# Optimization experiments

Hardware: AMD Instinct MI355X
Metric: run time of the kernel (lower is better)

The kernel has to match this reference:

```python
import jax, jax.numpy as jnp
import numpy as np

B, T, C, NH = 8, 1024, 768, 12
HD = C // NH


def setup_inputs() -> dict:
    key = jax.random.key(0)
    k1, k2, k3, k4, k5 = jax.random.split(key, 5)
    s = 0.02
    return {
        "x": jax.random.normal(k1, (B, T, C), dtype=jnp.float32),
        "w_attn": jax.random.normal(k2, (C, 3 * C), dtype=jnp.float32) * s,
        "b_attn": jax.random.normal(k3, (3 * C,), dtype=jnp.float32) * s,
        "w_proj": jax.random.normal(k4, (C, C), dtype=jnp.float32) * s,
        "b_proj": jax.random.normal(k5, (C,), dtype=jnp.float32) * s,
    }


def reference(x, w_attn, b_attn, w_proj, b_proj):
    Bv, Tv, Cv = x.shape
    # fused QKV projection
    qkv = jnp.einsum('btc,cd->btd', x, w_attn) + b_attn  # [B,T,3C]
    q, k, v = jnp.split(qkv, 3, axis=-1)
    # [B, NH, T, HD]
    q = q.reshape(Bv, Tv, NH, HD).transpose(0, 2, 1, 3)
    k = k.reshape(Bv, Tv, NH, HD).transpose(0, 2, 1, 3)
    v = v.reshape(Bv, Tv, NH, HD).transpose(0, 2, 1, 3)
    scale = 1.0 / np.sqrt(HD).astype(np.float32)
    att = jnp.einsum('bhqd,bhkd->bhqk', q, k) * scale  # [B,NH,T,T]
    causal = jnp.tril(jnp.ones((Tv, Tv), dtype=bool))
    att = jnp.where(causal, att, -jnp.inf)
    att = jax.nn.softmax(att, axis=-1)
    y = jnp.einsum('bhqk,bhkd->bhqd', att, v)  # [B,NH,T,HD]
    y = y.transpose(0, 2, 1, 3).reshape(Bv, Tv, Cv)
    return jnp.einsum('btc,cd->btd', y, w_proj) + b_proj
```

## Files before the change

kernel.cpp:

```cpp
#include <hip/hip_runtime.h>

constexpr int kB  = 8;
constexpr int kT  = 1024;
constexpr int kC  = 768;
constexpr int kNH = 12;
constexpr int kHD = 64;
constexpr int kM  = kB * kT;
constexpr int k3C = 3 * kC;

using bf16x8 = __attribute__((ext_vector_type(8))) __bf16;
using f32x4  = __attribute__((ext_vector_type(4))) float;

__device__ __forceinline__ float bf2f(unsigned short u) {
    union { unsigned int i; float f; } v;
    v.i = ((unsigned int)u) << 16;
    return v.f;
}

__device__ __forceinline__ unsigned short f2bf(float f) {
    union { float f; unsigned int u; } v; v.f = f;
    unsigned int r = v.u + 0x7fffu + ((v.u >> 16) & 1u);
    return (unsigned short)(r >> 16);
}

__device__ __forceinline__ void async16(const void* g, void* l) {
    __builtin_amdgcn_global_load_lds(
        (__attribute__((address_space(1))) void*)g,
        (__attribute__((address_space(3))) void*)l, 16, 0, 0);
}

__device__ __forceinline__ void wait_vm0() {
    __builtin_amdgcn_s_waitcnt(0x0F70);
}


__global__ __launch_bounds__(256) void cvt_bf16_kernel(
    const float* __restrict__ in, unsigned short* __restrict__ out)
{
    const int i = blockIdx.x * 256 + threadIdx.x;
    const float4 v = ((const float4*)in)[i];
    ushort4 o;
    o.x = f2bf(v.x); o.y = f2bf(v.y); o.z = f2bf(v.z); o.w = f2bf(v.w);
    ((ushort4*)out)[i] = o;
}

__global__ __launch_bounds__(256) void transpose_cvt_kernel(
    const float* __restrict__ W, unsigned short* __restrict__ Wt, int K, int N)
{
    __shared__ float tile[32][33];
    const int tx = threadIdx.x & 31, ty = threadIdx.x >> 5;
    const int n0 = blockIdx.x * 32, k0 = blockIdx.y * 32;
    #pragma unroll
    for (int i = 0; i < 4; ++i)
        tile[ty + i * 8][tx] = W[(size_t)(k0 + ty + i * 8) * N + n0 + tx];
    __syncthreads();
    #pragma unroll
    for (int i = 0; i < 4; ++i)
        Wt[(size_t)(n0 + ty + i * 8) * K + k0 + tx] = f2bf(tile[tx][ty + i * 8]);
}

__global__ __launch_bounds__(256) void vtrans_kernel(
    const unsigned short* __restrict__ qkv, unsigned short* __restrict__ VT)
{
    __shared__ unsigned short tile[64][72];
    const int tid = threadIdx.x;
    const int bh = blockIdx.x >> 4;
    const int b = bh / kNH, h = bh % kNH;
    const int tt = (blockIdx.x & 15) * 64;
    const int row = tid >> 2;
    const int c0  = (tid & 3) * 16;
    const unsigned short* src =
        qkv + (size_t)(b * kT + tt + row) * k3C + 2 * kC + h * kHD + c0;
    *(uint4*)&tile[row][c0]     = *(const uint4*)src;
    *(uint4*)&tile[row][c0 + 8] = *(const uint4*)(src + 8);
    __syncthreads();
    const int d  = tid >> 2;
    const int t8 = (tid & 3) * 16;
    unsigned short tmp[16];
    #pragma unroll
    for (int i = 0; i < 16; ++i) tmp[i] = tile[t8 + i][d];
    unsigned short* dst = VT + ((size_t)bh * kHD + d) * kT + tt + t8;
    *(uint4*)dst       = *(uint4*)&tmp[0];
    *(uint4*)(dst + 8) = *(uint4*)&tmp[8];
}

template<bool OUT_BF16>
__global__ __launch_bounds__(256) void gemm_mfma_kernel(
    const unsigned short* __restrict__ A, int lda,
    const unsigned short* __restrict__ Bt,
    const float* __restrict__ bias,
    void* __restrict__ outv, int N, int K)
{
    alignas(16) __shared__ unsigned short As[16 * 512];
    alignas(16) __shared__ unsigned short Bs[16 * 512];

    const int tid  = threadIdx.x;
    const int w    = tid >> 6;
    const int lane = tid & 63;
    const int wr = w >> 1, wc = w & 1;
    const int m0 = blockIdx.y * 128, n0 = blockIdx.x * 128;

    const int fr = lane & 15;
    const int fk = (lane >> 4) * 8;

    f32x4 acc[4][4];
    #pragma unroll
    for (int i = 0; i < 4; ++i)
        #pragma unroll
        for (int j = 0; j < 4; ++j) {
            f32x4 z = {0.f, 0.f, 0.f, 0.f};
            acc[i][j] = z;
        }

    for (int kt = 0; kt < K; kt += 64) {
        #pragma unroll
        for (int t = 0; t < 4; ++t) {
            const int fa = w * 4 + t;
            const int ki = fa >> 3, si = fa & 7;
            const unsigned short* ga =
                A + (size_t)(m0 + si * 16 + fr) * lda + kt + ki * 32 + fk;
            async16(ga, &As[fa * 512]);
            const unsigned short* gb =
                Bt + (size_t)(n0 + si * 16 + fr) * K + kt + ki * 32 + fk;
            async16(gb, &Bs[fa * 512]);
        }
        wait_vm0();
        __syncthreads();

        #pragma unroll
        for (int ki = 0; ki < 2; ++ki) {
            bf16x8 a[4], b[4];
            #pragma unroll
            for (int i = 0; i < 4; ++i)
                a[i] = *(const bf16x8*)&As[(ki * 8 + wr * 4 + i) * 512 + lane * 8];
            #pragma unroll
            for (int j = 0; j < 4; ++j)
                b[j] = *(const bf16x8*)&Bs[(ki * 8 + wc * 4 + j) * 512 + lane * 8];
            #pragma unroll
            for (int i = 0; i < 4; ++i)
                #pragma unroll
                for (int j = 0; j < 4; ++j)
                    acc[i][j] = __builtin_amdgcn_mfma_f32_16x16x32_bf16(
                        a[i], b[j], acc[i][j], 0, 0, 0);
        }
        __syncthreads();
    }

    const int quad  = lane >> 4;
    const int col16 = lane & 15;
    float biasv[4];
    #pragma unroll
    for (int j = 0; j < 4; ++j)
        biasv[j] = bias[n0 + wc * 64 + j * 16 + col16];

    #pragma unroll
    for (int i = 0; i < 4; ++i) {
        #pragma unroll
        for (int r = 0; r < 4; ++r) {
            const int row = m0 + wr * 64 + i * 16 + quad * 4 + r;
            #pragma unroll
            for (int j = 0; j < 4; ++j) {
                const int col = n0 + wc * 64 + j * 16 + col16;
                const float v = acc[i][j][r] + biasv[j];
                if (OUT_BF16)
                    ((unsigned short*)outv)[(size_t)row * N + col] = f2bf(v);
                else
                    ((float*)outv)[(size_t)row * N + col] = v;
            }
        }
    }
}

__global__ __launch_bounds__(256) void attn_mfma_kernel(
    const unsigned short* __restrict__ qkv,
    const unsigned short* __restrict__ VT,
    unsigned short* __restrict__ y)
{
    alignas(16) __shared__ unsigned short Qf[8 * 512];
    alignas(16) __shared__ unsigned short Kf[8 * 512];
    alignas(16) __shared__ unsigned short Vf[8 * 512];
    alignas(16) __shared__ unsigned short Pf[8 * 512];

    const int tid  = threadIdx.x;
    const int w    = tid >> 6;
    const int lane = tid & 63;
    const int quad = lane >> 4, l15 = lane & 15;
    const int bh = blockIdx.x >> 4;
    const int b  = bh / kNH, h = bh % kNH;
    const int t0 = (15 - (blockIdx.x & 15)) * 64;

    {
        const unsigned short* g0 =
            qkv + (size_t)(b * kT + t0 + w * 16 + l15) * k3C + h * kHD + quad * 8;
        async16(g0,      &Qf[(w * 2 + 0) * 512]);
        async16(g0 + 32, &Qf[(w * 2 + 1) * 512]);
    }

    float m_run[4], l_run[4];
    f32x4 acc_o[4];
    #pragma unroll
    for (int r = 0; r < 4; ++r) { m_run[r] = -INFINITY; l_run[r] = 0.f; }
    #pragma unroll
    for (int n = 0; n < 4; ++n) {
        f32x4 z = {0.f, 0.f, 0.f, 0.f};
        acc_o[n] = z;
    }

    const int nchunks = t0 / 64 + 1;
    for (int c = 0; c < nchunks; ++c) {
        const int kbase = c * 64;
        __syncthreads();
        {
            const unsigned short* gk = qkv +
                (size_t)(b * kT + kbase + w * 16 + l15) * k3C + kC + h * kHD + quad * 8;
            async16(gk,      &Kf[(w * 2 + 0) * 512]);
            async16(gk + 32, &Kf[(w * 2 + 1) * 512]);
            const unsigned short* gv = VT +
                ((size_t)bh * kHD + w * 16 + l15) * kT + kbase + quad * 8;
            async16(gv,      &Vf[(w * 2 + 0) * 512]);
            async16(gv + 32, &Vf[(w * 2 + 1) * 512]);
        }
        wait_vm0();
        __syncthreads();

        f32x4 acc_s[4];
        #pragma unroll
        for (int k = 0; k < 4; ++k) {
            f32x4 z = {0.f, 0.f, 0.f, 0.f};
            acc_s[k] = z;
        }
        const bf16x8 aq0 = *(const bf16x8*)&Qf[(w * 2 + 0) * 512 + lane * 8];
        const bf16x8 aq1 = *(const bf16x8*)&Qf[(w * 2 + 1) * 512 + lane * 8];
        #pragma unroll
        for (int ksub = 0; ksub < 4; ++ksub) {
            const bf16x8 bk0 = *(const bf16x8*)&Kf[(ksub * 2 + 0) * 512 + lane * 8];
            const bf16x8 bk1 = *(const bf16x8*)&Kf[(ksub * 2 + 1) * 512 + lane * 8];
            acc_s[ksub] = __builtin_amdgcn_mfma_f32_16x16x32_bf16(
                aq0, bk0, acc_s[ksub], 0, 0, 0);
            acc_s[ksub] = __builtin_amdgcn_mfma_f32_16x16x32_bf16(
                aq1, bk1, acc_s[ksub], 0, 0, 0);
        }

        float sv[4][4];
        #pragma unroll
        for (int ksub = 0; ksub < 4; ++ksub)
            #pragma unroll
            for (int r = 0; r < 4; ++r)
                sv[ksub][r] = acc_s[ksub][r] * 0.125f;
        if (kbase == t0) {
            const int qrow = t0 + w * 16 + quad * 4;
            #pragma unroll
            for (int ksub = 0; ksub < 4; ++ksub) {
                const int key = kbase + ksub * 16 + l15;
                #pragma unroll
                for (int r = 0; r < 4; ++r)
                    if (key > qrow + r) sv[ksub][r] = -INFINITY;
            }
        }

        float alpha[4];
        #pragma unroll
        for (int r = 0; r < 4; ++r) {
            float mx = fmaxf(fmaxf(sv[0][r], sv[1][r]), fmaxf(sv[2][r], sv[3][r]));
            mx = fmaxf(mx, __shfl_xor(mx, 1));
            mx = fmaxf(mx, __shfl_xor(mx, 2));
            mx = fmaxf(mx, __shfl_xor(mx, 4));
            mx = fmaxf(mx, __shfl_xor(mx, 8));
            const float m_new = fmaxf(m_run[r], mx);
            alpha[r] = __expf(m_run[r] - m_new);
            float ps = 0.f;
            #pragma unroll
            for (int ksub = 0; ksub < 4; ++ksub) {
                sv[ksub][r] = __expf(sv[ksub][r] - m_new);
                ps += sv[ksub][r];
            }
            ps += __shfl_xor(ps, 1);
            ps += __shfl_xor(ps, 2);
            ps += __shfl_xor(ps, 4);
            ps += __shfl_xor(ps, 8);
            l_run[r] = l_run[r] * alpha[r] + ps;
            m_run[r] = m_new;
        }

        #pragma unroll
        for (int ksub = 0; ksub < 4; ++ksub) {
            const int key = ksub * 16 + l15;
            #pragma unroll
            for (int r = 0; r < 4; ++r) {
                const int lp = quad * 4 + r + ((key & 31) >> 3) * 16;
                Pf[(w * 2 + (key >> 5)) * 512 + lp * 8 + (key & 7)] =
                    f2bf(sv[ksub][r]);
            }
        }

        #pragma unroll
        for (int n = 0; n < 4; ++n)
            #pragma unroll
            for (int r = 0; r < 4; ++r)
                acc_o[n][r] *= alpha[r];
        const bf16x8 ap0 = *(const bf16x8*)&Pf[(w * 2 + 0) * 512 + lane * 8];
        const bf16x8 ap1 = *(const bf16x8*)&Pf[(w * 2 + 1) * 512 + lane * 8];
        #pragma unroll
        for (int nsub = 0; nsub < 4; ++nsub) {
            const bf16x8 bv0 = *(const bf16x8*)&Vf[(nsub * 2 + 0) * 512 + lane * 8];
            const bf16x8 bv1 = *(const bf16x8*)&Vf[(nsub * 2 + 1) * 512 + lane * 8];
            acc_o[nsub] = __builtin_amdgcn_mfma_f32_16x16x32_bf16(
                ap0, bv0, acc_o[nsub], 0, 0, 0);
            acc_o[nsub] = __builtin_amdgcn_mfma_f32_16x16x32_bf16(
                ap1, bv1, acc_o[nsub], 0, 0, 0);
        }
    }

    float inv[4];
    #pragma unroll
    for (int r = 0; r < 4; ++r) inv[r] = 1.0f / l_run[r];
    #pragma unroll
    for (int nsub = 0; nsub < 4; ++nsub)
        #pragma unroll
        for (int r = 0; r < 4; ++r)
            y[(size_t)(b * kT + t0 + w * 16 + quad * 4 + r) * kC +
              h * kHD + nsub * 16 + l15] = f2bf(acc_o[nsub][r] * inv[r]);
}

extern "C" void kernel_launch(void* const* d_in, const int* in_sizes, int n_in,
                              void* d_out, int out_size, void* d_ws, size_t ws_size,
                              hipStream_t stream) {
    const float* x      = (const float*)d_in[0];
    const float* w_attn = (const float*)d_in[1];
    const float* b_attn = (const float*)d_in[2];
    const float* w_proj = (const float*)d_in[3];
    const float* b_proj = (const float*)d_in[4];
    float* out = (float*)d_out;

    unsigned short* xb     = (unsigned short*)d_ws;
    unsigned short* VT     = xb;
    unsigned short* wattnT = xb     + (size_t)kM * kC;
    unsigned short* wprojT = wattnT + (size_t)k3C * kC;
    unsigned short* qkv    = wprojT + (size_t)kC * kC;
    unsigned short* yb     = qkv    + (size_t)kM * k3C;

    cvt_bf16_kernel<<<(kM * kC) / (4 * 256), 256, 0, stream>>>(x, xb);
    transpose_cvt_kernel<<<dim3(k3C / 32, kC / 32), 256, 0, stream>>>(
        w_attn, wattnT, kC, k3C);
    transpose_cvt_kernel<<<dim3(kC / 32, kC / 32), 256, 0, stream>>>(
        w_proj, wprojT, kC, kC);

    gemm_mfma_kernel<true><<<dim3(k3C / 128, kM / 128), 256, 0, stream>>>(
        xb, kC, wattnT, b_attn, qkv, k3C, kC);

    vtrans_kernel<<<kB * kNH * (kT / 64), 256, 0, stream>>>(qkv, VT);

    attn_mfma_kernel<<<kB * kNH * (kT / 64), 256, 0, stream>>>(qkv, VT, yb);

    gemm_mfma_kernel<false><<<dim3(kC / 128, kM / 128), 256, 0, stream>>>(
        yb, kC, wprojT, b_proj, out, kC, kC);
}
```

Measured before the change: 283.5 us.

## Double-buffer K/V tiles in attention kernel and keep Q in registers

The attention kernel now keeps two K and V buffers in shared memory and issues the async load for the next 64-key chunk right after the barrier, so it overlaps with the current chunk's MFMA and softmax work. Q is loaded once into registers, reusing the P buffer as staging, which removes the Q shared array and keeps LDS usage near its old size. This hides global-load latency behind compute and drops one barrier per iteration. The cost is more LDS per block, which may lower occupancy, and reuse of Pf relies on each wave reading only its own Q region before writing P.

```diff
diff --git a/kernel.cpp b/kernel.cpp
--- a/kernel.cpp
+++ b/kernel.cpp
@@ -176,9 +176,8 @@
     const unsigned short* __restrict__ VT,
     unsigned short* __restrict__ y)
 {
-    alignas(16) __shared__ unsigned short Qf[8 * 512];
-    alignas(16) __shared__ unsigned short Kf[8 * 512];
-    alignas(16) __shared__ unsigned short Vf[8 * 512];
+    alignas(16) __shared__ unsigned short Kf[2][8 * 512];
+    alignas(16) __shared__ unsigned short Vf[2][8 * 512];
     alignas(16) __shared__ unsigned short Pf[8 * 512];
 
     const int tid  = threadIdx.x;
@@ -188,13 +187,29 @@
     const int bh = blockIdx.x >> 4;
     const int b  = bh / kNH, h = bh % kNH;
     const int t0 = (15 - (blockIdx.x & 15)) * 64;
-
+    const int nchunks = t0 / 64 + 1;
+
+    auto stage = [&](int bufi, int kbase) {
+        const unsigned short* gk = qkv +
+            (size_t)(b * kT + kbase + w * 16 + l15) * k3C + kC + h * kHD + quad * 8;
+        async16(gk,      &Kf[bufi][(w * 2 + 0) * 512]);
+        async16(gk + 32, &Kf[bufi][(w * 2 + 1) * 512]);
+        const unsigned short* gv = VT +
+            ((size_t)bh * kHD + w * 16 + l15) * kT + kbase + quad * 8;
+        async16(gv,      &Vf[bufi][(w * 2 + 0) * 512]);
+        async16(gv + 32, &Vf[bufi][(w * 2 + 1) * 512]);
+    };
+
+    stage(0, 0);
     {
         const unsigned short* g0 =
             qkv + (size_t)(b * kT + t0 + w * 16 + l15) * k3C + h * kHD + quad * 8;
-        async16(g0,      &Qf[(w * 2 + 0) * 512]);
-        async16(g0 + 32, &Qf[(w * 2 + 1) * 512]);
-    }
+        async16(g0,      &Pf[(w * 2 + 0) * 512]);
+        async16(g0 + 32, &Pf[(w * 2 + 1) * 512]);
+    }
+    wait_vm0();
+    const bf16x8 aq0 = *(const bf16x8*)&Pf[(w * 2 + 0) * 512 + lane * 8];
+    const bf16x8 aq1 = *(const bf16x8*)&Pf[(w * 2 + 1) * 512 + lane * 8];
 
     float m_run[4], l_run[4];
     f32x4 acc_o[4];
@@ -206,22 +221,12 @@
         acc_o[n] = z;
     }
 
-    const int nchunks = t0 / 64 + 1;
     for (int c = 0; c < nchunks; ++c) {
         const int kbase = c * 64;
-        __syncthreads();
-        {
-            const unsigned short* gk = qkv +
-                (size_t)(b * kT + kbase + w * 16 + l15) * k3C + kC + h * kHD + quad * 8;
-            async16(gk,      &Kf[(w * 2 + 0) * 512]);
-            async16(gk + 32, &Kf[(w * 2 + 1) * 512]);
-            const unsigned short* gv = VT +
-                ((size_t)bh * kHD + w * 16 + l15) * kT + kbase + quad * 8;
-            async16(gv,      &Vf[(w * 2 + 0) * 512]);
-            async16(gv + 32, &Vf[(w * 2 + 1) * 512]);
-        }
+        const int buf = c & 1;
         wait_vm0();
         __syncthreads();
+        if (c + 1 < nchunks) stage(1 - buf, kbase + 64);
 
         f32x4 acc_s[4];
         #pragma unroll
@@ -229,12 +234,12 @@
             f32x4 z = {0.f, 0.f, 0.f, 0.f};
             acc_s[k] = z;
         }
-        const bf16x8 aq0 = *(const bf16x8*)&Qf[(w * 2 + 0) * 512 + lane * 8];
-        const bf16x8 aq1 = *(const bf16x8*)&Qf[(w * 2 + 1) * 512 + lane * 8];
         #pragma unroll
         for (int ksub = 0; ksub < 4; ++ksub) {
-            const bf16x8 bk0 = *(const bf16x8*)&Kf[(ksub * 2 + 0) * 512 + lane * 8];
-            const bf16x8 bk1 = *(const bf16x8*)&Kf[(ksub * 2 + 1) * 512 + lane * 8];
+            const bf16x8 bk0 =
+                *(const bf16x8*)&Kf[buf][(ksub * 2 + 0) * 512 + lane * 8];
+            const bf16x8 bk1 =
+                *(const bf16x8*)&Kf[buf][(ksub * 2 + 1) * 512 + lane * 8];
             acc_s[ksub] = __builtin_amdgcn_mfma_f32_16x16x32_bf16(
                 aq0, bk0, acc_s[ksub], 0, 0, 0);
             acc_s[ksub] = __builtin_amdgcn_mfma_f32_16x16x32_bf16(
@@ -302,8 +307,10 @@
         const bf16x8 ap1 = *(const bf16x8*)&Pf[(w * 2 + 1) * 512 + lane * 8];
         #pragma unroll
         for (int nsub = 0; nsub < 4; ++nsub) {
-            const bf16x8 bv0 = *(const bf16x8*)&Vf[(nsub * 2 + 0) * 512 + lane * 8];
-            const bf16x8 bv1 = *(const bf16x8*)&Vf[(nsub * 2 + 1) * 512 + lane * 8];
+            const bf16x8 bv0 =
+                *(const bf16x8*)&Vf[buf][(nsub * 2 + 0) * 512 + lane * 8];
+            const bf16x8 bv1 =
+                *(const bf16x8*)&Vf[buf][(nsub * 2 + 1) * 512 + lane * 8];
             acc_o[nsub] = __builtin_amdgcn_mfma_f32_16x16x32_bf16(
                 ap0, bv0, acc_o[nsub], 0, 0, 0);
             acc_o[nsub] = __builtin_amdgcn_mfma_f32_16x16x32_bf16(
```

New measurement: 275.0 us. 3.0% less time.
